# Kernel tuning notes

Measured on AMD Instinct MI355X. Metric: run time of the kernel, lower is better.

Reference implementation:

```python
import jax, jax.numpy as jnp
import numpy as np
from jax import lax

KH, KW = 9, 9
FC_DIM = 1024
C_RED = FC_DIM // 8  # 128
EPS = 1e-5


def conv_bn_relu(x, w, gamma, beta):
    # 3x3 conv, stride 1, pad 1 (NCHW / OIHW), then batch-stat BN + ReLU
    y = lax.conv_general_dilated(x, w, (1, 1), ((1, 1), (1, 1)),
                                 dimension_numbers=('NCHW', 'OIHW', 'NCHW'))
    mean = y.mean(axis=(0, 2, 3))
    var = y.var(axis=(0, 2, 3))
    y = (y - mean[None, :, None, None]) * lax.rsqrt(var + EPS)[None, :, None, None]
    y = y * gamma[None, :, None, None] + beta[None, :, None, None]
    return jnp.maximum(y, 0.0)


def local_weighting(feat, atten, kH, kW):
    # feat: [B,C,H,W]; atten: [B,H,W,kH*kW]
    # out[b,c,h,w] = sum_k atten[b,h,w,k] * feat_padded[b,c,h+dh_k,w+dw_k]
    B, C, H, W = feat.shape
    ph, pw = kH // 2, kW // 2
    fp = jnp.pad(feat, ((0, 0), (0, 0), (ph, ph), (pw, pw)))
    out = jnp.zeros_like(feat)
    k = 0
    for dh in range(kH):
        for dw in range(kW):
            out = out + fp[:, :, dh:dh + H, dw:dw + W] * atten[:, None, :, :, k]
            k += 1
    return out


def setup_inputs() -> dict:
    key = jax.random.key(0)
    ks = jax.random.split(key, 12)
    B, H, W = 4, 64, 64
    sc1 = 1.0 / np.sqrt(FC_DIM * 9)
    sc5 = 1.0 / np.sqrt(C_RED * 9)
    return {
        'low_key': jax.random.normal(ks[0], (B, FC_DIM, H, W), jnp.float32),
        'low_nonkey': jax.random.normal(ks[1], (B, FC_DIM, H, W), jnp.float32),
        'local_atten': jax.random.uniform(ks[2], (B, H, W, KH * KW), jnp.float32),
        'w1': jax.random.normal(ks[3], (C_RED, FC_DIM, 3, 3), jnp.float32) * sc1,
        'g1': jnp.ones((C_RED,), jnp.float32),
        'b1': jnp.zeros((C_RED,), jnp.float32),
        'w4': jax.random.normal(ks[4], (C_RED, FC_DIM, 3, 3), jnp.float32) * sc1,
        'g4': jnp.ones((C_RED,), jnp.float32),
        'b4': jnp.zeros((C_RED,), jnp.float32),
        'w5': jax.random.normal(ks[5], (C_RED, C_RED, 3, 3), jnp.float32) * sc5,
        'g5': jnp.ones((C_RED,), jnp.float32),
        'b5': jnp.zeros((C_RED,), jnp.float32),
        'fc1_w': jax.random.normal(ks[6], (10, C_RED), jnp.float32) * (1.0 / np.sqrt(C_RED)),
        'fc1_b': jnp.zeros((10,), jnp.float32),
        'fc2_w': jax.random.normal(ks[7], (1, 10), jnp.float32) * (1.0 / np.sqrt(10.0)),
        'fc2_b': jnp.zeros((1,), jnp.float32),
    }


def reference(low_key, low_nonkey, local_atten,
              w1, g1, b1, w4, g4, b4, w5, g5, b5,
              fc1_w, fc1_b, fc2_w, fc2_b):
    lk = conv_bn_relu(low_key, w1, g1, b1)          # [B,128,H,W]
    trans = local_weighting(lk, local_atten, KH, KW)
    lnk = conv_bn_relu(low_nonkey, w4, g4, b4)
    out = trans - lnk
    out = conv_bn_relu(out, w5, g5, b5)
    out = out.mean(axis=(2, 3))                      # adaptive avg pool to 1x1 -> [B,128]
    out = out @ fc1_w.T + fc1_b
    out = out @ fc2_w.T + fc2_b                      # [B,1]
    return out
```

## Files before the change

kernel.cpp:

```cpp
#include <hip/hip_runtime.h>
#include <hip/hip_bf16.h>


#define B_ 4
#define CM_ 128

typedef __attribute__((ext_vector_type(8))) short short8;
typedef __attribute__((ext_vector_type(4))) float floatx4;
typedef __attribute__((address_space(3))) unsigned lds_as;
typedef __attribute__((address_space(1))) const unsigned glb_as;

__device__ inline short f2bf(float f) {
  union { float f; unsigned u; } v; v.f = f;
  unsigned r = v.u + 0x7fff + ((v.u >> 16) & 1);
  return (short)(r >> 16);
}
__device__ inline float bf2f(unsigned short u) {
  union { unsigned u; float f; } v; v.u = ((unsigned)u) << 16;
  return v.f;
}

__device__ __forceinline__ void kb_tail() {
  asm volatile("s_waitcnt vmcnt(0)" ::: "memory");
  __builtin_amdgcn_s_barrier();
  asm volatile("" ::: "memory");
}

template <int KB>
__global__ void xprep_kernel(const float* __restrict__ x, short* __restrict__ xt) {
  int kb = blockIdx.x >> 4, rg = blockIdx.x & 15;
  int b = blockIdx.y;
  int row = rg * 4 + (threadIdx.x >> 6);
  int col = threadIdx.x & 63;
  const float* xs = x + (((size_t)b * (KB * 32) + kb * 32) * 64 + row) * 64 + col;
  short* xd = xt + ((((size_t)b * KB + kb) * 64 + row) * 64 + col) * 32;
  int sw = (col >> 1) & 3;
#pragma unroll
  for (int u = 0; u < 4; u++) {
    short8 pk;
#pragma unroll
    for (int j = 0; j < 8; j++) pk[j] = f2bf(xs[(size_t)(u * 8 + j) * 4096]);
    *(short8*)(xd + (u ^ sw) * 8) = pk;
  }
}

__global__ void prep1_kernel(const float* __restrict__ x1,
                             const float* __restrict__ w1, const float* __restrict__ w4,
                             const float* __restrict__ w5, const float* __restrict__ atten,
                             short* __restrict__ xt, short* __restrict__ wf1,
                             short* __restrict__ wf4, short* __restrict__ wf5,
                             float* __restrict__ att_t, float* __restrict__ yz) {
  __shared__ float tile[5184];
  int bx = blockIdx.x, tid = threadIdx.x;
  if (bx < 2048) {
    int b = bx & 3, t = bx >> 2;
    int kb = t >> 4, rg = t & 15;
    int row = rg * 4 + (tid >> 6), col = tid & 63;
    const float* xs = x1 + (((size_t)b * 1024 + kb * 32) * 64 + row) * 64 + col;
    short* xd = xt + ((((size_t)b * 32 + kb) * 64 + row) * 64 + col) * 32;
    int sw = (col >> 1) & 3;
#pragma unroll
    for (int u = 0; u < 4; u++) {
      short8 pk;
#pragma unroll
      for (int j = 0; j < 8; j++) pk[j] = f2bf(xs[(size_t)(u * 8 + j) * 4096]);
      *(short8*)(xd + (u ^ sw) * 8) = pk;
    }
    return;
  }
  bx -= 2048;
  if (bx < 1024) {
    const float* w = bx < 512 ? w1 : w4;
    short* wf = bx < 512 ? wf1 : wf4;
    int idx = (bx & 511) * 256 + tid;
    int oc = idx >> 10, ic = idx & 1023;
    int kb = ic >> 5, icb = ic & 31, quad = icb >> 3, j = icb & 7;
    int m = oc >> 4, n16 = oc & 15, lane = quad * 16 + n16;
    const float* wp = w + ((size_t)oc * 1024 + ic) * 9;
    short* base = wf + (size_t)kb * 36864 + lane * 8 + j;
#pragma unroll
    for (int r = 0; r < 3; r++)
#pragma unroll
      for (int s = 0; s < 3; s++)
        base[(size_t)r * 12288 + (s * 8 + m) * 512] = f2bf(wp[r * 3 + s]);
    return;
  }
  bx -= 1024;
  if (bx < 64) {
    int idx = bx * 256 + tid;
    int oc = idx >> 7, ic = idx & 127;
    int kb = ic >> 5, icb = ic & 31, quad = icb >> 3, j = icb & 7;
    int m = oc >> 4, n16 = oc & 15, lane = quad * 16 + n16;
    const float* wp = w5 + ((size_t)oc * 128 + ic) * 9;
    short* base = wf5 + (size_t)kb * 36864 + lane * 8 + j;
#pragma unroll
    for (int r = 0; r < 3; r++)
#pragma unroll
      for (int s = 0; s < 3; s++)
        base[(size_t)r * 12288 + (s * 8 + m) * 512] = f2bf(wp[r * 3 + s]);
    return;
  }
  bx -= 64;
  if (bx < 256) {
    int b = bx >> 6;
    int p0 = (bx & 63) * 64;
    const float* src = atten + ((size_t)b * 4096 + p0) * 81;
    for (int e = tid; e < 5184; e += 256) tile[e] = src[e];
    __syncthreads();
    for (int f = tid; f < 5184; f += 256) {
      int k = f >> 6, w_ = f & 63;
      att_t[((size_t)b * 81 + k) * 4096 + p0 + w_] = tile[w_ * 81 + k];
    }
    return;
  }
  bx -= 256;
  ((float4*)yz)[(size_t)bx * 256 + tid] = make_float4(0.f, 0.f, 0.f, 0.f);
}

template <int KQ, bool ATOMIC>
__global__ __launch_bounds__(256, 2)
void convm_kernel(const short* __restrict__ xt, const short* __restrict__ wf,
                  float* __restrict__ ya, float* __restrict__ yb, int KBtot) {
  __shared__ __attribute__((aligned(16))) short smem[16384];
  int tid = threadIdx.x, lane = tid & 63, wv = tid >> 6;
  int n16 = lane & 15, quad = lane >> 4;
  int pg = blockIdx.x;
  int b = pg >> 5, h0 = (pg & 31) * 2;
  int kb0 = blockIdx.y * KQ;
  int mh = wv & 1, nh = wv >> 1;
  float* yo = ATOMIC ? ya : (blockIdx.y ? yb : ya);

  if (h0 == 0)
    for (int i = tid; i < 1024; i += 256) {
      ((int*)smem)[i] = 0;
      ((int*)(smem + 8192))[i] = 0;
    }
  if (h0 == 62)
    for (int i = tid; i < 1024; i += 256) {
      ((int*)(smem + 3 * 2048))[i] = 0;
      ((int*)(smem + 8192 + 3 * 2048))[i] = 0;
    }

  int xrow = h0 - 1 + wv;
  int xw = __builtin_amdgcn_readfirstlane((xrow >= 0 && xrow < 64) ? 1 : 0);
  const short* wfa = wf + (size_t)kb0 * 36864 + ((mh * 4) * 64 + lane) * 8;

  int boff[3][4];
#pragma unroll
  for (int sp = 0; sp < 3; sp++)
#pragma unroll
    for (int n = 0; n < 4; n++) {
      int c = n * 16 + n16 + sp - 1;
      int cc = c < 0 ? 0 : (c > 63 ? 63 : c);
      boff[sp][n] = cc * 32 + (quad ^ ((cc >> 1) & 3)) * 8;
    }
  bool bz00 = (n16 == 0), bz32 = (n16 == 15);

  floatx4 acc[4][4];
#pragma unroll
  for (int i = 0; i < 4; i++)
#pragma unroll
    for (int n = 0; n < 4; n++) acc[i][n] = (floatx4){0.f, 0.f, 0.f, 0.f};

  short8 AA[4], AB[4];

  if (xw) {
    const short* xs = xt + ((((size_t)b * KBtot + kb0) * 64 + xrow) * 64) * 32 + lane * 8;
    short* xd = smem + wv * 2048 + lane * 8;
#pragma unroll
    for (int t = 0; t < 4; t++)
      __builtin_amdgcn_global_load_lds((glb_as*)(xs + t * 512), (lds_as*)(xd + t * 512),
                                       16, 0, 0);
  }
#pragma unroll
  for (int i = 0; i < 4; i++) AA[i] = *(const short8*)(wfa + i * 512);
  asm volatile("s_waitcnt lgkmcnt(0)" ::: "memory");
  kb_tail();

#define PH(QV, E, ACUR, ANXT, DONP, DOX, XB, DOTAIL)                                 \
  {                                                                                  \
    constexpr int rr_ = (E) / 3, sp_ = (E) % 3;                                      \
    if (DONP) {                                                                      \
      const short* ap_ = wfa + (size_t)(9 * (QV) + (E) + 1) * 4096;                  \
      _Pragma("unroll")                                                              \
      for (int i = 0; i < 4; i++) ANXT[i] = *(const short8*)(ap_ + i * 512);         \
    }                                                                                \
    if ((DOX) && xw) {                                                               \
      const short* xs_ = xt +                                                        \
          ((((size_t)b * KBtot + kb0 + (QV) + 1) * 64 + xrow) * 64) * 32 + lane * 8; \
      short* xd_ = smem + (XB) * 8192 + wv * 2048 + lane * 8;                        \
      _Pragma("unroll")                                                              \
      for (int t = 0; t < 4; t++)                                                    \
        __builtin_amdgcn_global_load_lds((glb_as*)(xs_ + t * 512),                   \
                                         (lds_as*)(xd_ + t * 512), 16, 0, 0);        \
    }                                                                                \
    const short* sxr_ = smem + ((QV) & 1) * 8192 + (nh + rr_) * 2048;                \
    short8 bf_[4];                                                                   \
    _Pragma("unroll")                                                                \
    for (int n = 0; n < 4; n++) {                                                    \
      short8 bv = *(const short8*)(sxr_ + boff[sp_][n]);                             \
      if ((n == 0 && sp_ == 0) || (n == 3 && sp_ == 2)) {                            \
        short8 zz = {0, 0, 0, 0, 0, 0, 0, 0};                                        \
        bv = ((sp_ == 0) ? bz00 : bz32) ? zz : bv;                                   \
      }                                                                              \
      bf_[n] = bv;                                                                   \
    }                                                                                \
    __builtin_amdgcn_s_setprio(1);                                                   \
    _Pragma("unroll")                                                                \
    for (int n = 0; n < 4; n++)                                                      \
      _Pragma("unroll")                                                              \
      for (int i = 0; i < 4; i++)                                                    \
        acc[i][n] =                                                                  \
            __builtin_amdgcn_mfma_f32_16x16x32_bf16(ACUR[i], bf_[n], acc[i][n], 0, 0, 0); \
    __builtin_amdgcn_s_setprio(0);                                                   \
    if (DOTAIL) kb_tail();                                                           \
  }

  const int NDQ = KQ / 2;
  for (int dq = 0; dq < NDQ; ++dq) {
    int q0 = 2 * dq, q1 = q0 + 1;
    bool last = (dq == NDQ - 1);
    PH(q0, 0, AA, AB, true, true, 1, false)
    PH(q0, 1, AB, AA, true, false, 0, false)
    PH(q0, 2, AA, AB, true, false, 0, false)
    PH(q0, 3, AB, AA, true, false, 0, false)
    PH(q0, 4, AA, AB, true, false, 0, false)
    PH(q0, 5, AB, AA, true, false, 0, false)
    PH(q0, 6, AA, AB, true, false, 0, false)
    PH(q0, 7, AB, AA, true, false, 0, false)
    PH(q0, 8, AA, AB, true, false, 0, true)
    PH(q1, 0, AB, AA, true, !last, 0, false)
    PH(q1, 1, AA, AB, true, false, 0, false)
    PH(q1, 2, AB, AA, true, false, 0, false)
    PH(q1, 3, AA, AB, true, false, 0, false)
    PH(q1, 4, AB, AA, true, false, 0, false)
    PH(q1, 5, AA, AB, true, false, 0, false)
    PH(q1, 6, AB, AA, true, false, 0, false)
    PH(q1, 7, AA, AB, true, false, 0, false)
    PH(q1, 8, AB, AA, !last, false, 0, !last)
  }
#undef PH

  int orow = h0 + nh;
#pragma unroll
  for (int i = 0; i < 4; i++)
#pragma unroll
    for (int n = 0; n < 4; n++)
#pragma unroll
      for (int rg = 0; rg < 4; rg++) {
        int oc = mh * 64 + i * 16 + quad * 4 + rg;
        size_t gi = (((size_t)b * CM_ + oc) * 64 + orow) * 64 + n * 16 + n16;
        if (ATOMIC)
          atomicAdd(&yo[gi], acc[i][n][rg]);
        else
          yo[gi] = acc[i][n][rg];
      }
}

__global__ void bnstats2_kernel(const float* __restrict__ y1, const float* __restrict__ g1,
                                const float* __restrict__ b1, float2* __restrict__ s1,
                                const float* __restrict__ y4, const float* __restrict__ g4,
                                const float* __restrict__ b4, float2* __restrict__ s4) {
  const float* y = blockIdx.y ? y4 : y1;
  const float* g = blockIdx.y ? g4 : g1;
  const float* bt = blockIdx.y ? b4 : b1;
  float2* scsh = blockIdx.y ? s4 : s1;
  int c = blockIdx.x;
  int tid = threadIdx.x;
  float s = 0.f, s2 = 0.f;
  for (int b = 0; b < B_; b++) {
    const float4* p = (const float4*)(y + ((size_t)(b * CM_) + c) * 4096);
    for (int i = tid; i < 1024; i += 256) {
      float4 v = p[i];
      s += v.x + v.y + v.z + v.w;
      s2 += v.x * v.x + v.y * v.y + v.z * v.z + v.w * v.w;
    }
  }
  for (int off = 32; off > 0; off >>= 1) {
    s += __shfl_down(s, off);
    s2 += __shfl_down(s2, off);
  }
  __shared__ float rs[4], rq[4];
  if ((tid & 63) == 0) { rs[tid >> 6] = s; rq[tid >> 6] = s2; }
  __syncthreads();
  if (tid == 0) {
    float S = rs[0] + rs[1] + rs[2] + rs[3];
    float Q = rq[0] + rq[1] + rq[2] + rq[3];
    float mean = S * (1.f / 16384.f);
    float var = Q * (1.f / 16384.f) - mean * mean;
    float sc = g[c] * rsqrtf(var + 1e-5f);
    scsh[c] = make_float2(sc, bt[c] - mean * sc);
  }
}

__global__ void bnstats_s2_kernel(const float* __restrict__ ya, const float* __restrict__ yb,
                                  const float* __restrict__ g, const float* __restrict__ bt,
                                  float2* __restrict__ scsh) {
  int c = blockIdx.x;
  int tid = threadIdx.x;
  float s = 0.f, s2 = 0.f;
  for (int b = 0; b < B_; b++) {
    const float4* p = (const float4*)(ya + ((size_t)(b * CM_) + c) * 4096);
    const float4* q = (const float4*)(yb + ((size_t)(b * CM_) + c) * 4096);
    for (int i = tid; i < 1024; i += 256) {
      float4 v = p[i], w = q[i];
      float a0 = v.x + w.x, a1 = v.y + w.y, a2 = v.z + w.z, a3 = v.w + w.w;
      s += a0 + a1 + a2 + a3;
      s2 += a0 * a0 + a1 * a1 + a2 * a2 + a3 * a3;
    }
  }
  for (int off = 32; off > 0; off >>= 1) {
    s += __shfl_down(s, off);
    s2 += __shfl_down(s2, off);
  }
  __shared__ float rs[4], rq[4];
  if ((tid & 63) == 0) { rs[tid >> 6] = s; rq[tid >> 6] = s2; }
  __syncthreads();
  if (tid == 0) {
    float S = rs[0] + rs[1] + rs[2] + rs[3];
    float Q = rq[0] + rq[1] + rq[2] + rq[3];
    float mean = S * (1.f / 16384.f);
    float var = Q * (1.f / 16384.f) - mean * mean;
    float sc = g[c] * rsqrtf(var + 1e-5f);
    scsh[c] = make_float2(sc, bt[c] - mean * sc);
  }
}

__global__ __launch_bounds__(256, 2)
void localw_kernel(const float* __restrict__ y1, const float2* __restrict__ scsh1,
                   const float* __restrict__ y4, const float2* __restrict__ scsh4,
                   const float* __restrict__ att_t, short* __restrict__ xt5) {
  __shared__ unsigned short lkb[16][12][72];
  int bx = blockIdx.x;
  int b = bx >> 4, h0 = (bx & 15) * 4;
  int cg = blockIdx.y;
  int tid = threadIdx.x;
  int lane = tid & 63;
  int wv = tid >> 6;

  for (int e = tid; e < 16 * 12 * 72; e += 256) {
    int c_l = e / (12 * 72);
    int rem = e % (12 * 72);
    int gri = rem / 72, j = rem % 72;
    int row = h0 - 4 + gri, col = j - 4;
    float v = 0.f;
    if (row >= 0 && row < 64 && col >= 0 && col < 64) {
      float2 ss = scsh1[cg * 16 + c_l];
      v = fmaxf(0.f, y1[((size_t)(b * CM_) + cg * 16 + c_l) * 4096 + row * 64 + col] * ss.x + ss.y);
    }
    lkb[c_l][gri][j] = (unsigned short)f2bf(v);
  }
  __syncthreads();

  float acc[4][4];
#pragma unroll
  for (int cc = 0; cc < 4; cc++)
#pragma unroll
    for (int h_i = 0; h_i < 4; h_i++) acc[cc][h_i] = 0.f;

  const float* ab = att_t + (size_t)b * 81 * 4096 + h0 * 64 + lane;

#pragma unroll
  for (int gri = 0; gri < 12; ++gri) {
    float win[4][9];
#pragma unroll
    for (int cc = 0; cc < 4; ++cc)
#pragma unroll
      for (int dw = 0; dw < 9; ++dw)
        win[cc][dw] = bf2f(lkb[wv * 4 + cc][gri][lane + dw]);
#pragma unroll
    for (int h_i = 0; h_i < 4; ++h_i) {
      int r = gri - h_i;
      if (r < 0 || r > 8) continue;
      const float* ap = ab + (size_t)(r * 9) * 4096 + h_i * 64;
      float a[9];
#pragma unroll
      for (int dw = 0; dw < 9; ++dw) a[dw] = ap[(size_t)dw * 4096];
#pragma unroll
      for (int cc = 0; cc < 4; ++cc)
#pragma unroll
        for (int dw = 0; dw < 9; ++dw)
          acc[cc][h_i] = fmaf(a[dw], win[cc][dw], acc[cc][h_i]);
    }
  }

#pragma unroll
  for (int cc = 0; cc < 4; ++cc) {
    int c = cg * 16 + wv * 4 + cc;
    float2 ss4 = scsh4[c];
    int icb = c & 31;
    int uu = (icb >> 3) ^ ((lane >> 1) & 3);
#pragma unroll
    for (int h_i = 0; h_i < 4; ++h_i) {
      int h = h0 + h_i;
      size_t gi = ((size_t)(b * CM_) + c) * 4096 + h * 64 + lane;
      float lnk = fmaxf(0.f, y4[gi] * ss4.x + ss4.y);
      float dv = acc[cc][h_i] - lnk;
      xt5[((((size_t)b * 4 + (c >> 5)) * 64 + h) * 64 + lane) * 32 + uu * 8 + (icb & 7)] =
          f2bf(dv);
    }
  }
}

__global__ void pool_kernel(const float* __restrict__ ya, const float* __restrict__ yb,
                            const float2* __restrict__ scsh, float* __restrict__ pooled) {
  int bc = blockIdx.x;
  int c = bc & 127;
  float2 ss = scsh[c];
  const float4* p = (const float4*)(ya + (size_t)bc * 4096);
  const float4* q = (const float4*)(yb + (size_t)bc * 4096);
  float s = 0.f;
  for (int i = threadIdx.x; i < 1024; i += 256) {
    float4 v = p[i], w = q[i];
    s += fmaxf(0.f, (v.x + w.x) * ss.x + ss.y) + fmaxf(0.f, (v.y + w.y) * ss.x + ss.y) +
         fmaxf(0.f, (v.z + w.z) * ss.x + ss.y) + fmaxf(0.f, (v.w + w.w) * ss.x + ss.y);
  }
  for (int off = 32; off > 0; off >>= 1) s += __shfl_down(s, off);
  __shared__ float rs[4];
  if ((threadIdx.x & 63) == 0) rs[threadIdx.x >> 6] = s;
  __syncthreads();
  if (threadIdx.x == 0) pooled[bc] = (rs[0] + rs[1] + rs[2] + rs[3]) * (1.f / 4096.f);
}

__global__ void fc_kernel(const float* __restrict__ pooled, const float* __restrict__ fc1w,
                          const float* __restrict__ fc1b, const float* __restrict__ fc2w,
                          const float* __restrict__ fc2b, float* __restrict__ out) {
  int lane = threadIdx.x;
  float p[B_][10];
#pragma unroll
  for (int b = 0; b < B_; b++)
#pragma unroll
    for (int j = 0; j < 10; j++) p[b][j] = 0.f;
  for (int c = lane; c < CM_; c += 64) {
#pragma unroll
    for (int b = 0; b < B_; b++) {
      float pv = pooled[b * CM_ + c];
#pragma unroll
      for (int j = 0; j < 10; j++) p[b][j] = fmaf(pv, fc1w[j * CM_ + c], p[b][j]);
    }
  }
  for (int off = 32; off > 0; off >>= 1)
#pragma unroll
    for (int b = 0; b < B_; b++)
#pragma unroll
      for (int j = 0; j < 10; j++) p[b][j] += __shfl_down(p[b][j], off);
  if (lane == 0) {
    for (int b = 0; b < B_; b++) {
      float o = fc2b[0];
      for (int j = 0; j < 10; j++) o += fc2w[j] * (p[b][j] + fc1b[j]);
      out[b] = o;
    }
  }
}

extern "C" void kernel_launch(void* const* d_in, const int* in_sizes, int n_in,
                              void* d_out, int out_size, void* d_ws, size_t ws_size,
                              hipStream_t stream) {
  const float* low_key    = (const float*)d_in[0];
  const float* low_nonkey = (const float*)d_in[1];
  const float* atten      = (const float*)d_in[2];
  const float* w1  = (const float*)d_in[3];
  const float* g1  = (const float*)d_in[4];
  const float* b1  = (const float*)d_in[5];
  const float* w4  = (const float*)d_in[6];
  const float* g4  = (const float*)d_in[7];
  const float* b4  = (const float*)d_in[8];
  const float* w5  = (const float*)d_in[9];
  const float* g5  = (const float*)d_in[10];
  const float* b5  = (const float*)d_in[11];
  const float* fc1w = (const float*)d_in[12];
  const float* fc1b = (const float*)d_in[13];
  const float* fc2w = (const float*)d_in[14];
  const float* fc2b = (const float*)d_in[15];

  char* w8 = (char*)d_ws;
  short* wf1   = (short*)w8;
  short* wf4   = (short*)(w8 + 2359296);
  short* wf5   = (short*)(w8 + 4718592);
  float* att_t = (float*)(w8 + 5308416);
  short* xt    = (short*)(w8 + 10616832);
  float* y1    = (float*)(w8 + 44171264);
  float* y4    = (float*)(w8 + 52559872);
  float2* scsh1 = (float2*)(w8 + 60948480);
  float2* scsh4 = scsh1 + CM_;
  float2* scsh5 = scsh4 + CM_;
  float* pooled = (float*)(scsh5 + CM_);
  short* xt5 = xt;
  float* out = (float*)d_out;

  prep1_kernel<<<7488, 256, 0, stream>>>(low_key, w1, w4, w5, atten,
                                         xt, wf1, wf4, wf5, att_t, y1);
  convm_kernel<8, true><<<dim3(128, 4), 256, 0, stream>>>(xt, wf1, y1, y1, 32);
  xprep_kernel<32><<<dim3(512, 4), 256, 0, stream>>>(low_nonkey, xt);
  convm_kernel<8, true><<<dim3(128, 4), 256, 0, stream>>>(xt, wf4, y4, y4, 32);
  bnstats2_kernel<<<dim3(128, 2), 256, 0, stream>>>(y1, g1, b1, scsh1, y4, g4, b4, scsh4);
  localw_kernel<<<dim3(64, 8), 256, 0, stream>>>(y1, scsh1, y4, scsh4, att_t, xt5);
  convm_kernel<2, false><<<dim3(128, 2), 256, 0, stream>>>(xt5, wf5, y1, y4, 4);
  bnstats_s2_kernel<<<128, 256, 0, stream>>>(y1, y4, g5, b5, scsh5);
  pool_kernel<<<512, 256, 0, stream>>>(y1, y4, scsh5, pooled);
  fc_kernel<<<1, 64, 0, stream>>>(pooled, fc1w, fc1b, fc2w, fc2b, out);
}
```

Measured before the change: 384.3 us.

## Retile conv to 4 output rows per block and fuse BN stats with pooling

The implicit-GEMM conv kernel now computes 4 output rows and all 128 output channels per block, one row per wave. It stages 6 input rows in LDS per K block instead of 4, so each staged input row and each weight fragment is reused across more outputs. The K split for the large convs goes from 4 to 8 chunks, keeping the grid at 512 blocks, at the cost of more atomic adds into the output. The accumulator count doubles to 8x4 per thread, which raises register pressure. Separately, the layer-5 BN statistics and the avg-pool kernels are merged into one kernel, saving a launch and a pass over the conv outputs.

```diff
diff --git a/kernel.cpp b/kernel.cpp
--- a/kernel.cpp
+++ b/kernel.cpp
@@ -121,29 +121,50 @@
 __global__ __launch_bounds__(256, 2)
 void convm_kernel(const short* __restrict__ xt, const short* __restrict__ wf,
                   float* __restrict__ ya, float* __restrict__ yb, int KBtot) {
-  __shared__ __attribute__((aligned(16))) short smem[16384];
+  __shared__ __attribute__((aligned(16))) short smem[24576];
   int tid = threadIdx.x, lane = tid & 63, wv = tid >> 6;
   int n16 = lane & 15, quad = lane >> 4;
   int pg = blockIdx.x;
-  int b = pg >> 5, h0 = (pg & 31) * 2;
+  int b = pg >> 4, h0 = (pg & 15) * 4;
   int kb0 = blockIdx.y * KQ;
-  int mh = wv & 1, nh = wv >> 1;
   float* yo = ATOMIC ? ya : (blockIdx.y ? yb : ya);
 
   if (h0 == 0)
     for (int i = tid; i < 1024; i += 256) {
       ((int*)smem)[i] = 0;
-      ((int*)(smem + 8192))[i] = 0;
-    }
-  if (h0 == 62)
+      ((int*)(smem + 12288))[i] = 0;
+    }
+  if (h0 == 60)
     for (int i = tid; i < 1024; i += 256) {
-      ((int*)(smem + 3 * 2048))[i] = 0;
-      ((int*)(smem + 8192 + 3 * 2048))[i] = 0;
-    }
-
-  int xrow = h0 - 1 + wv;
-  int xw = __builtin_amdgcn_readfirstlane((xrow >= 0 && xrow < 64) ? 1 : 0);
-  const short* wfa = wf + (size_t)kb0 * 36864 + ((mh * 4) * 64 + lane) * 8;
+      ((int*)(smem + 5 * 2048))[i] = 0;
+      ((int*)(smem + 12288 + 5 * 2048))[i] = 0;
+    }
+
+  int xrow1 = h0 - 1 + wv;
+  int xrow2 = h0 + 3 + wv;
+  int xw1 = __builtin_amdgcn_readfirstlane((xrow1 >= 0 && xrow1 < 64) ? 1 : 0);
+  int xw2 = __builtin_amdgcn_readfirstlane((wv < 2 && xrow2 < 64) ? 1 : 0);
+
+  auto dma_x = [&](int kb, int bufi) {
+    if (xw1) {
+      const short* xs = xt + ((((size_t)b * KBtot + kb) * 64 + xrow1) * 64) * 32 + lane * 8;
+      short* xd = smem + bufi * 12288 + wv * 2048 + lane * 8;
+#pragma unroll
+      for (int t = 0; t < 4; t++)
+        __builtin_amdgcn_global_load_lds((glb_as*)(xs + t * 512), (lds_as*)(xd + t * 512),
+                                         16, 0, 0);
+    }
+    if (xw2) {
+      const short* xs = xt + ((((size_t)b * KBtot + kb) * 64 + xrow2) * 64) * 32 + lane * 8;
+      short* xd = smem + bufi * 12288 + (4 + wv) * 2048 + lane * 8;
+#pragma unroll
+      for (int t = 0; t < 4; t++)
+        __builtin_amdgcn_global_load_lds((glb_as*)(xs + t * 512), (lds_as*)(xd + t * 512),
+                                         16, 0, 0);
+    }
+  };
+
+  const short* wfa = wf + (size_t)kb0 * 36864 + lane * 8;
 
   int boff[3][4];
 #pragma unroll
@@ -156,45 +177,28 @@
     }
   bool bz00 = (n16 == 0), bz32 = (n16 == 15);
 
-  floatx4 acc[4][4];
-#pragma unroll
-  for (int i = 0; i < 4; i++)
+  floatx4 acc[8][4];
+#pragma unroll
+  for (int i = 0; i < 8; i++)
 #pragma unroll
     for (int n = 0; n < 4; n++) acc[i][n] = (floatx4){0.f, 0.f, 0.f, 0.f};
 
-  short8 AA[4], AB[4];
-
-  if (xw) {
-    const short* xs = xt + ((((size_t)b * KBtot + kb0) * 64 + xrow) * 64) * 32 + lane * 8;
-    short* xd = smem + wv * 2048 + lane * 8;
-#pragma unroll
-    for (int t = 0; t < 4; t++)
-      __builtin_amdgcn_global_load_lds((glb_as*)(xs + t * 512), (lds_as*)(xd + t * 512),
-                                       16, 0, 0);
-  }
-#pragma unroll
-  for (int i = 0; i < 4; i++) AA[i] = *(const short8*)(wfa + i * 512);
+  short8 AX[4], AY[4];
+
+  dma_x(kb0, 0);
+#pragma unroll
+  for (int j = 0; j < 4; j++) AX[j] = *(const short8*)(wfa + j * 512);
   asm volatile("s_waitcnt lgkmcnt(0)" ::: "memory");
   kb_tail();
 
-#define PH(QV, E, ACUR, ANXT, DONP, DOX, XB, DOTAIL)                                 \
+#define TAP(E, DOXV, SKIP2)                                                          \
   {                                                                                  \
     constexpr int rr_ = (E) / 3, sp_ = (E) % 3;                                      \
-    if (DONP) {                                                                      \
-      const short* ap_ = wfa + (size_t)(9 * (QV) + (E) + 1) * 4096;                  \
-      _Pragma("unroll")                                                              \
-      for (int i = 0; i < 4; i++) ANXT[i] = *(const short8*)(ap_ + i * 512);         \
-    }                                                                                \
-    if ((DOX) && xw) {                                                               \
-      const short* xs_ = xt +                                                        \
-          ((((size_t)b * KBtot + kb0 + (QV) + 1) * 64 + xrow) * 64) * 32 + lane * 8; \
-      short* xd_ = smem + (XB) * 8192 + wv * 2048 + lane * 8;                        \
-      _Pragma("unroll")                                                              \
-      for (int t = 0; t < 4; t++)                                                    \
-        __builtin_amdgcn_global_load_lds((glb_as*)(xs_ + t * 512),                   \
-                                         (lds_as*)(xd_ + t * 512), 16, 0, 0);        \
-    }                                                                                \
-    const short* sxr_ = smem + ((QV) & 1) * 8192 + (nh + rr_) * 2048;                \
+    const short* ap_ = wfa + (size_t)(9 * q + (E)) * 4096;                           \
+    _Pragma("unroll")                                                                \
+    for (int j = 0; j < 4; j++) AY[j] = *(const short8*)(ap_ + (4 + j) * 512);       \
+    if (DOXV) dma_x(kb0 + q + 1, bufc ^ 1);                                          \
+    const short* sxr_ = smem + bufc * 12288 + (wv + rr_) * 2048;                     \
     short8 bf_[4];                                                                   \
     _Pragma("unroll")                                                                \
     for (int n = 0; n < 4; n++) {                                                    \
@@ -209,46 +213,50 @@
     _Pragma("unroll")                                                                \
     for (int n = 0; n < 4; n++)                                                      \
       _Pragma("unroll")                                                              \
-      for (int i = 0; i < 4; i++)                                                    \
-        acc[i][n] =                                                                  \
-            __builtin_amdgcn_mfma_f32_16x16x32_bf16(ACUR[i], bf_[n], acc[i][n], 0, 0, 0); \
+      for (int j = 0; j < 4; j++)                                                    \
+        acc[j][n] =                                                                  \
+            __builtin_amdgcn_mfma_f32_16x16x32_bf16(AX[j], bf_[n], acc[j][n], 0, 0, 0); \
     __builtin_amdgcn_s_setprio(0);                                                   \
-    if (DOTAIL) kb_tail();                                                           \
-  }
-
-  const int NDQ = KQ / 2;
-  for (int dq = 0; dq < NDQ; ++dq) {
-    int q0 = 2 * dq, q1 = q0 + 1;
-    bool last = (dq == NDQ - 1);
-    PH(q0, 0, AA, AB, true, true, 1, false)
-    PH(q0, 1, AB, AA, true, false, 0, false)
-    PH(q0, 2, AA, AB, true, false, 0, false)
-    PH(q0, 3, AB, AA, true, false, 0, false)
-    PH(q0, 4, AA, AB, true, false, 0, false)
-    PH(q0, 5, AB, AA, true, false, 0, false)
-    PH(q0, 6, AA, AB, true, false, 0, false)
-    PH(q0, 7, AB, AA, true, false, 0, false)
-    PH(q0, 8, AA, AB, true, false, 0, true)
-    PH(q1, 0, AB, AA, true, !last, 0, false)
-    PH(q1, 1, AA, AB, true, false, 0, false)
-    PH(q1, 2, AB, AA, true, false, 0, false)
-    PH(q1, 3, AA, AB, true, false, 0, false)
-    PH(q1, 4, AB, AA, true, false, 0, false)
-    PH(q1, 5, AA, AB, true, false, 0, false)
-    PH(q1, 6, AB, AA, true, false, 0, false)
-    PH(q1, 7, AA, AB, true, false, 0, false)
-    PH(q1, 8, AB, AA, !last, false, 0, !last)
-  }
-#undef PH
-
-  int orow = h0 + nh;
-#pragma unroll
-  for (int i = 0; i < 4; i++)
+    if (!(SKIP2)) {                                                                  \
+      const short* an_ = wfa + (size_t)(9 * q + (E) + 1) * 4096;                     \
+      _Pragma("unroll")                                                              \
+      for (int j = 0; j < 4; j++) AX[j] = *(const short8*)(an_ + j * 512);           \
+    }                                                                                \
+    __builtin_amdgcn_s_setprio(1);                                                   \
+    _Pragma("unroll")                                                                \
+    for (int n = 0; n < 4; n++)                                                      \
+      _Pragma("unroll")                                                              \
+      for (int j = 0; j < 4; j++)                                                    \
+        acc[4 + j][n] =                                                              \
+            __builtin_amdgcn_mfma_f32_16x16x32_bf16(AY[j], bf_[n], acc[4 + j][n], 0, 0, 0); \
+    __builtin_amdgcn_s_setprio(0);                                                   \
+  }
+
+  for (int q = 0; q < KQ; ++q) {
+    int bufc = q & 1;
+    bool lastq = (q == KQ - 1);
+    bool dox0 = !lastq;
+    TAP(0, dox0, false)
+    TAP(1, false, false)
+    TAP(2, false, false)
+    TAP(3, false, false)
+    TAP(4, false, false)
+    TAP(5, false, false)
+    TAP(6, false, false)
+    TAP(7, false, false)
+    TAP(8, false, lastq)
+    if (!lastq) kb_tail();
+  }
+#undef TAP
+
+  int orow = h0 + wv;
+#pragma unroll
+  for (int i = 0; i < 8; i++)
 #pragma unroll
     for (int n = 0; n < 4; n++)
 #pragma unroll
       for (int rg = 0; rg < 4; rg++) {
-        int oc = mh * 64 + i * 16 + quad * 4 + rg;
+        int oc = i * 16 + quad * 4 + rg;
         size_t gi = (((size_t)b * CM_ + oc) * 64 + orow) * 64 + n * 16 + n16;
         if (ATOMIC)
           atomicAdd(&yo[gi], acc[i][n][rg]);
@@ -293,9 +301,9 @@
   }
 }
 
-__global__ void bnstats_s2_kernel(const float* __restrict__ ya, const float* __restrict__ yb,
-                                  const float* __restrict__ g, const float* __restrict__ bt,
-                                  float2* __restrict__ scsh) {
+__global__ void bnpool_kernel(const float* __restrict__ ya, const float* __restrict__ yb,
+                              const float* __restrict__ g, const float* __restrict__ bt,
+                              float* __restrict__ pooled) {
   int c = blockIdx.x;
   int tid = threadIdx.x;
   float s = 0.f, s2 = 0.f;
@@ -314,6 +322,7 @@
     s2 += __shfl_down(s2, off);
   }
   __shared__ float rs[4], rq[4];
+  __shared__ float2 ss_sh;
   if ((tid & 63) == 0) { rs[tid >> 6] = s; rq[tid >> 6] = s2; }
   __syncthreads();
   if (tid == 0) {
@@ -322,8 +331,33 @@
     float mean = S * (1.f / 16384.f);
     float var = Q * (1.f / 16384.f) - mean * mean;
     float sc = g[c] * rsqrtf(var + 1e-5f);
-    scsh[c] = make_float2(sc, bt[c] - mean * sc);
-  }
+    ss_sh = make_float2(sc, bt[c] - mean * sc);
+  }
+  __syncthreads();
+  float2 ss = ss_sh;
+  float pb[B_];
+#pragma unroll
+  for (int b = 0; b < B_; b++) pb[b] = 0.f;
+  for (int b = 0; b < B_; b++) {
+    const float4* p = (const float4*)(ya + ((size_t)(b * CM_) + c) * 4096);
+    const float4* q = (const float4*)(yb + ((size_t)(b * CM_) + c) * 4096);
+    for (int i = tid; i < 1024; i += 256) {
+      float4 v = p[i], w = q[i];
+      pb[b] += fmaxf(0.f, (v.x + w.x) * ss.x + ss.y) + fmaxf(0.f, (v.y + w.y) * ss.x + ss.y) +
+               fmaxf(0.f, (v.z + w.z) * ss.x + ss.y) + fmaxf(0.f, (v.w + w.w) * ss.x + ss.y);
+    }
+  }
+  for (int off = 32; off > 0; off >>= 1)
+#pragma unroll
+    for (int b = 0; b < B_; b++) pb[b] += __shfl_down(pb[b], off);
+  __shared__ float pbs[4][B_];
+  if ((tid & 63) == 0)
+#pragma unroll
+    for (int b = 0; b < B_; b++) pbs[tid >> 6][b] = pb[b];
+  __syncthreads();
+  if (tid < B_)
+    pooled[tid * CM_ + c] =
+        (pbs[0][tid] + pbs[1][tid] + pbs[2][tid] + pbs[3][tid]) * (1.f / 4096.f);
 }
 
 __global__ __launch_bounds__(256, 2)
@@ -400,26 +434,6 @@
           f2bf(dv);
     }
   }
-}
-
-__global__ void pool_kernel(const float* __restrict__ ya, const float* __restrict__ yb,
-                            const float2* __restrict__ scsh, float* __restrict__ pooled) {
-  int bc = blockIdx.x;
-  int c = bc & 127;
-  float2 ss = scsh[c];
-  const float4* p = (const float4*)(ya + (size_t)bc * 4096);
-  const float4* q = (const float4*)(yb + (size_t)bc * 4096);
-  float s = 0.f;
-  for (int i = threadIdx.x; i < 1024; i += 256) {
-    float4 v = p[i], w = q[i];
-    s += fmaxf(0.f, (v.x + w.x) * ss.x + ss.y) + fmaxf(0.f, (v.y + w.y) * ss.x + ss.y) +
-         fmaxf(0.f, (v.z + w.z) * ss.x + ss.y) + fmaxf(0.f, (v.w + w.w) * ss.x + ss.y);
-  }
-  for (int off = 32; off > 0; off >>= 1) s += __shfl_down(s, off);
-  __shared__ float rs[4];
-  if ((threadIdx.x & 63) == 0) rs[threadIdx.x >> 6] = s;
-  __syncthreads();
-  if (threadIdx.x == 0) pooled[bc] = (rs[0] + rs[1] + rs[2] + rs[3]) * (1.f / 4096.f);
 }
 
 __global__ void fc_kernel(const float* __restrict__ pooled, const float* __restrict__ fc1w,
@@ -490,13 +504,12 @@
 
   prep1_kernel<<<7488, 256, 0, stream>>>(low_key, w1, w4, w5, atten,
                                          xt, wf1, wf4, wf5, att_t, y1);
-  convm_kernel<8, true><<<dim3(128, 4), 256, 0, stream>>>(xt, wf1, y1, y1, 32);
+  convm_kernel<4, true><<<dim3(64, 8), 256, 0, stream>>>(xt, wf1, y1, y1, 32);
   xprep_kernel<32><<<dim3(512, 4), 256, 0, stream>>>(low_nonkey, xt);
-  convm_kernel<8, true><<<dim3(128, 4), 256, 0, stream>>>(xt, wf4, y4, y4, 32);
+  convm_kernel<4, true><<<dim3(64, 8), 256, 0, stream>>>(xt, wf4, y4, y4, 32);
   bnstats2_kernel<<<dim3(128, 2), 256, 0, stream>>>(y1, g1, b1, scsh1, y4, g4, b4, scsh4);
   localw_kernel<<<dim3(64, 8), 256, 0, stream>>>(y1, scsh1, y4, scsh4, att_t, xt5);
-  convm_kernel<2, false><<<dim3(128, 2), 256, 0, stream>>>(xt5, wf5, y1, y4, 4);
-  bnstats_s2_kernel<<<128, 256, 0, stream>>>(y1, y4, g5, b5, scsh5);
-  pool_kernel<<<512, 256, 0, stream>>>(y1, y4, scsh5, pooled);
+  convm_kernel<2, false><<<dim3(64, 2), 256, 0, stream>>>(xt5, wf5, y1, y4, 4);
+  bnpool_kernel<<<128, 256, 0, stream>>>(y1, y4, g5, b5, pooled);
   fc_kernel<<<1, 64, 0, stream>>>(pooled, fc1w, fc1b, fc2w, fc2b, out);
 }
```

After: 446.4 us. 1.16x slower.
